# Kernel tuning notes

Hardware: AMD Instinct MI355X
Metric: run time of the kernel (lower is better)

The kernel has to match this reference:

```python
import jax, jax.numpy as jnp
import numpy as np

B, S, H, NH = 2, 2048, 1024, 16
P = H // NH

def setup_inputs() -> dict:
    key = jax.random.key(0)
    k1, k2, k3, k4 = jax.random.split(key, 4)
    x = jax.random.normal(k1, (B, S, H), dtype=jnp.float32)
    mask = jax.random.randint(k2, (B, S), 0, 2).astype(jnp.int32)
    # weights: (num_heads, 3, hidden, partial) -- the leading singleton dim of the
    # torch parameter is pure broadcast, dropped here.
    W = jax.random.normal(k3, (NH, 3, H, P), dtype=jnp.float32) * (1.0 / np.sqrt(H))
    Wl = jax.random.normal(k4, (H, H), dtype=jnp.float32) * (1.0 / np.sqrt(H))
    bl = jnp.zeros((H,), dtype=jnp.float32)
    return {"x": x, "mask": mask, "W": W, "Wl": Wl, "bl": bl}

def reference(x, mask, W, Wl, bl):
    nh, _, h, p = W.shape
    scale = 1.0 / np.sqrt(p)
    # kvq[b, t, n, s, p]; t=0 keys, t=1 values, t=2 queries (unbind order in source)
    kvq = jnp.einsum('bsh,nthp->btnsp', x, W)
    keys, values, queries = kvq[:, 0], kvq[:, 1], kvq[:, 2]  # each [B, NH, S, P]
    # NOTE: source computes keys @ queries^T -> scores[b,n,i,j] = k_i . q_j
    scores = jnp.einsum('bnip,bnjp->bnij', keys, queries) * scale
    # mask==0 zeroes out the LAST axis (query positions), exactly as the fancy-index write
    scores = jnp.where(mask[:, None, None, :] == 0, jnp.float32(-1e12), scores)
    # softmax over dim=2 (key axis), as in the source (Softmax(dim=2))
    w = jax.nn.softmax(scores, axis=2)
    out = jnp.einsum('bnij,bnjp->bnip', w, values)  # [B, NH, S, P]
    b, _, s, _ = out.shape
    hidden = out.transpose(0, 2, 1, 3).reshape(b, s, nh * p)  # concat heads
    return hidden @ Wl.T + bl
```

## Files before the change

kernel.cpp:

```cpp
#include <hip/hip_runtime.h>

#define B_ 2
#define S_ 2048
#define H_ 1024
#define NH_ 16
#define P_ 64

using f32x4 = __attribute__((ext_vector_type(4))) float;
using i32x4 = __attribute__((ext_vector_type(4))) int;
using f16   = _Float16;
using f16x8 = __attribute__((ext_vector_type(8))) f16;
using f16x4 = __attribute__((ext_vector_type(4))) f16;

static __device__ __forceinline__ f16x8 ldh8(const f16* p) { return *(const f16x8*)p; }
static __device__ __forceinline__ f32x4 ld4f(const float* p) { return *(const f32x4*)p; }

static __device__ __forceinline__ f32x4 mm16(f16x8 a, f16x8 b, f32x4 c) {
  return __builtin_amdgcn_mfma_f32_16x16x32_f16(a, b, c, 0, 0, 0);
}

__global__ __launch_bounds__(256) void tw_kernel(
    const float* __restrict__ W, f16* __restrict__ WtH)
{
  __shared__ float T[64 * 65];
  const int tid = threadIdx.x;
  const int nt = blockIdx.x >> 4;
  const int h0 = (blockIdx.x & 15) * 64;
  const float* src = W + (size_t)nt * H_ * P_ + (size_t)h0 * P_;
  #pragma unroll
  for (int r = 0; r < 4; ++r) {
    int idx = tid + r * 256;
    int h = idx >> 4, p4 = (idx & 15) << 2;
    f32x4 v = ld4f(src + (size_t)h * P_ + p4);
    #pragma unroll
    for (int i = 0; i < 4; ++i) T[(p4 + i) * 65 + h] = v[i];
  }
  __syncthreads();
  f16* dh = WtH + (size_t)nt * P_ * H_;
  #pragma unroll
  for (int r = 0; r < 4; ++r) {
    int idx = tid + r * 256;
    int p = idx >> 4, h4 = (idx & 15) << 2;
    f16x4 hv;
    #pragma unroll
    for (int i = 0; i < 4; ++i) hv[i] = (f16)T[p * 65 + h4 + i];
    *(f16x4*)(dh + (size_t)p * H_ + h0 + h4) = hv;
  }
}

__global__ __launch_bounds__(256) void swl_kernel(
    const float* __restrict__ Wl, f16* __restrict__ WlH)
{
  int idx = blockIdx.x * 256 + threadIdx.x;
  f32x4 v = ((const f32x4*)Wl)[idx];
  f16x4 h;
  #pragma unroll
  for (int i = 0; i < 4; ++i) h[i] = (f16)v[i];
  ((f16x4*)WlH)[idx] = h;
}

__global__ __launch_bounds__(256) void qkv_kernel(
    const float* __restrict__ x, const f16* __restrict__ WtH,
    f16* __restrict__ Kh, f16* __restrict__ Qh, f16* __restrict__ VTh)
{
  __shared__ f16 xls[2][64 * 64];

  int blk = blockIdx.x;
  const int st = blk & 31; blk >>= 5;
  const int n = blk & 15;
  const int b = blk >> 4;
  const int s0 = st * 64;
  const int tid = threadIdx.x;
  const int w = tid >> 6, lane = tid & 63, q = lane >> 4, fr = lane & 15;
  const int bn = b * NH_ + n;

  const int srow = tid >> 2, scc = tid & 3;
  const float* xsrc = x + ((size_t)b * S_ + s0 + srow) * H_ + 16 * scc;
  const int c0 = ((2 * scc) ^ (srow & 7)) * 8;
  const int c1 = ((2 * scc + 1) ^ (srow & 7)) * 8;

  auto stage = [&](int k0, int bs) {
    f32x4 v0 = ld4f(xsrc + k0),     v1 = ld4f(xsrc + k0 + 4);
    f32x4 v2 = ld4f(xsrc + k0 + 8), v3 = ld4f(xsrc + k0 + 12);
    f16x8 a, b2;
    #pragma unroll
    for (int e = 0; e < 4; ++e) {
      a[e] = (f16)v0[e];  a[e + 4] = (f16)v1[e];
      b2[e] = (f16)v2[e]; b2[e + 4] = (f16)v3[e];
    }
    *(f16x8*)&xls[bs][srow * 64 + c0] = a;
    *(f16x8*)&xls[bs][srow * 64 + c1] = b2;
  };

  const f16* WtK = WtH + ((size_t)(n * 3 + 0) * P_ + 16 * w + fr) * H_ + 8 * q;
  const f16* WtV = WtH + ((size_t)(n * 3 + 1) * P_ + 16 * w + fr) * H_ + 8 * q;
  const f16* WtQ = WtH + ((size_t)(n * 3 + 2) * P_ + 16 * w + fr) * H_ + 8 * q;

  f32x4 accK[4] = {}, accQ[4] = {}, accV[4] = {};

  stage(0, 0);
  for (int step = 0; step < 16; ++step) {
    __syncthreads();
    if (step < 15) stage((step + 1) * 64, (step + 1) & 1);
    const int bs = step & 1;
    const int k0 = step * 64;

    f16x8 xf[4][2];
    #pragma unroll
    for (int ss = 0; ss < 4; ++ss) {
      int row = 16 * ss + fr;
      #pragma unroll
      for (int ks = 0; ks < 2; ++ks) {
        int ch = ((q + 4 * ks) ^ (row & 7)) * 8;
        xf[ss][ks] = *(const f16x8*)&xls[bs][row * 64 + ch];
      }
    }
    f16x8 wk0 = ldh8(WtK + k0), wk1 = ldh8(WtK + k0 + 32);
    f16x8 wq0 = ldh8(WtQ + k0), wq1 = ldh8(WtQ + k0 + 32);
    f16x8 wv0 = ldh8(WtV + k0), wv1 = ldh8(WtV + k0 + 32);
    #pragma unroll
    for (int ss = 0; ss < 4; ++ss) {
      accK[ss] = mm16(wk0, xf[ss][0], accK[ss]);
      accK[ss] = mm16(wk1, xf[ss][1], accK[ss]);
      accQ[ss] = mm16(wq0, xf[ss][0], accQ[ss]);
      accQ[ss] = mm16(wq1, xf[ss][1], accQ[ss]);
      accV[ss] = mm16(xf[ss][0], wv0, accV[ss]);
      accV[ss] = mm16(xf[ss][1], wv1, accV[ss]);
    }
  }

  #pragma unroll
  for (int ss = 0; ss < 4; ++ss) {
    f16x4 hK, hQ;
    #pragma unroll
    for (int c = 0; c < 4; ++c) {
      hK[c] = (f16)accK[ss][c];
      hQ[c] = (f16)(accQ[ss][c] * 0.125f);
    }
    size_t off = ((size_t)bn * S_ + (s0 + 16 * ss + fr)) * P_ + 16 * w + 4 * q;
    *(f16x4*)(Kh + off) = hK;
    *(f16x4*)(Qh + off) = hQ;
  }
  #pragma unroll
  for (int ss = 0; ss < 4; ++ss) {
    f16x4 hV;
    #pragma unroll
    for (int c = 0; c < 4; ++c) hV[c] = (f16)accV[ss][c];
    size_t off = ((size_t)bn * P_ + (16 * w + fr)) * S_ + s0 + 16 * ss + 4 * q;
    *(f16x4*)(VTh + off) = hV;
  }
}

__global__ __launch_bounds__(256) void stats_kernel(
    const f16* __restrict__ Kh, const f16* __restrict__ Qh,
    float* __restrict__ csuminv)
{
  __shared__ float zbuf[2 * 64];
  const int tid = threadIdx.x;
  const int bid = blockIdx.x;
  const int j0 = (bid & 31) * 64;
  const int bn = bid >> 5;
  const int w = tid >> 6, lane = tid & 63, q = lane >> 4, fr = lane & 15;
  const int jb = 32 * (w & 1), ih = w >> 1, ib0 = 32 * ih;

  f16x8 qf[2][2];
  #pragma unroll
  for (int jt = 0; jt < 2; ++jt)
    #pragma unroll
    for (int ks = 0; ks < 2; ++ks)
      qf[jt][ks] = ldh8(Qh + ((size_t)bn * S_ + (j0 + jb + 16 * jt + fr)) * P_ + 8 * q + 32 * ks);

  f32x4 z[2] = {};
  f16x8 kA[2][2], kB[2][2];

  auto loadK = [&](f16x8 (&kf)[2][2], int i0) {
    #pragma unroll
    for (int it = 0; it < 2; ++it)
      #pragma unroll
      for (int ks = 0; ks < 2; ++ks)
        kf[it][ks] = ldh8(Kh + ((size_t)bn * S_ + (i0 + ib0 + 16 * it + fr)) * P_ + 8 * q + 32 * ks);
  };
  auto step = [&](f16x8 (&kf)[2][2]) {
    f32x4 sc[2][2] = {};
    #pragma unroll
    for (int ks = 0; ks < 2; ++ks)
      #pragma unroll
      for (int jt = 0; jt < 2; ++jt)
        #pragma unroll
        for (int it = 0; it < 2; ++it)
          sc[jt][it] = mm16(qf[jt][ks], kf[it][ks], sc[jt][it]);
    #pragma unroll
    for (int jt = 0; jt < 2; ++jt)
      #pragma unroll
      for (int c = 0; c < 4; ++c)
        z[jt][c] += __expf(sc[jt][0][c]) + __expf(sc[jt][1][c]);
  };

  loadK(kA, 0);
  for (int i0 = 0; i0 < S_; i0 += 128) {
    loadK(kB, i0 + 64);
    step(kA);
    loadK(kA, (i0 + 128) & (S_ - 1));
    step(kB);
  }

  #pragma unroll
  for (int msk = 1; msk <= 8; msk <<= 1)
    #pragma unroll
    for (int jt = 0; jt < 2; ++jt)
      #pragma unroll
      for (int c = 0; c < 4; ++c)
        z[jt][c] += __shfl_xor(z[jt][c], msk, 64);

  if (fr == 0) {
    #pragma unroll
    for (int jt = 0; jt < 2; ++jt)
      *(f32x4*)&zbuf[ih * 64 + jb + 16 * jt + 4 * q] = z[jt];
  }
  __syncthreads();
  if (tid < 64)
    csuminv[(size_t)bn * S_ + j0 + tid] = 1.0f / (zbuf[tid] + zbuf[64 + tid]);
}

__global__ __launch_bounds__(256) void scale_kernel(
    f16* __restrict__ VT, const float* __restrict__ csuminv,
    const int* __restrict__ mask, float* __restrict__ Cbuf)
{
  const int bid = blockIdx.x;
  const int bn = bid >> 4;
  const int b = bn >> 4;
  const int p = (bid & 15) * 4 + (threadIdx.x >> 6);
  const int lane = threadIdx.x & 63;
  f16* row = VT + ((size_t)bn * P_ + p) * S_;
  const float* zr = csuminv + (size_t)bn * S_;
  const int* mr = mask + (size_t)b * S_;
  float acc = 0.0f;
  #pragma unroll
  for (int k = 0; k < 4; ++k) {
    int s = (lane + 64 * k) * 8;
    f16x8 v = *(const f16x8*)(row + s);
    f32x4 z0 = ld4f(zr + s), z1 = ld4f(zr + s + 4);
    i32x4 m0 = *(const i32x4*)(mr + s), m1 = *(const i32x4*)(mr + s + 4);
    f16x8 o;
    #pragma unroll
    for (int e = 0; e < 4; ++e) {
      float fv = (float)v[e];
      if (m0[e] != 0) o[e] = (f16)(fv * z0[e]);
      else { o[e] = (f16)0.0f; acc += fv; }
      float fv2 = (float)v[e + 4];
      if (m1[e] != 0) o[e + 4] = (f16)(fv2 * z1[e]);
      else { o[e + 4] = (f16)0.0f; acc += fv2; }
    }
    *(f16x8*)(row + s) = o;
  }
  #pragma unroll
  for (int msk = 1; msk <= 32; msk <<= 1) acc += __shfl_xor(acc, msk, 64);
  if (lane == 0) Cbuf[bn * P_ + p] = acc * (1.0f / S_);
}

__global__ __launch_bounds__(256) void av_kernel(
    const f16* __restrict__ Kh, const f16* __restrict__ Qh,
    const f16* __restrict__ VT, const float* __restrict__ Cbuf,
    f16* __restrict__ hidh)
{
  __shared__ f16  elds[4][64 * 40];
  __shared__ float accl[64 * 68];
  const int tid = threadIdx.x;
  const int bid = blockIdx.x;
  const int i0 = (bid & 31) * 64;
  const int bn = bid >> 5;
  const int b = bn >> 4, n = bn & 15;
  const int w = tid >> 6, lane = tid & 63, q = lane >> 4, fr = lane & 15;
  f16* ew = &elds[w][0];

  f16x8 kf[4][2];
  #pragma unroll
  for (int it = 0; it < 4; ++it)
    #pragma unroll
    for (int ks = 0; ks < 2; ++ks)
      kf[it][ks] = ldh8(Kh + ((size_t)bn * S_ + (i0 + 16 * it + fr)) * P_ + 8 * q + 32 * ks);

  f32x4 opv[4][4] = {};

  for (int T = 0; T < S_ / 128; ++T) {
    const int j0 = T * 128 + w * 32;

    f16x8 aq[2][2];
    #pragma unroll
    for (int jt = 0; jt < 2; ++jt)
      #pragma unroll
      for (int ks = 0; ks < 2; ++ks)
        aq[jt][ks] = ldh8(Qh + ((size_t)bn * S_ + (j0 + 16 * jt + fr)) * P_ + 8 * q + 32 * ks);
    f16x8 va[4];
    #pragma unroll
    for (int pt = 0; pt < 4; ++pt)
      va[pt] = ldh8(VT + ((size_t)bn * P_ + (16 * pt + fr)) * S_ + j0 + 8 * q);

    #pragma unroll
    for (int it = 0; it < 4; ++it) {
      f32x4 s0 = {}, s1 = {};
      s0 = mm16(aq[0][0], kf[it][0], s0);
      s0 = mm16(aq[0][1], kf[it][1], s0);
      s1 = mm16(aq[1][0], kf[it][0], s1);
      s1 = mm16(aq[1][1], kf[it][1], s1);
      f16x4 e0, e1;
      #pragma unroll
      for (int c = 0; c < 4; ++c) {
        e0[c] = (f16)__expf(s0[c]);
        e1[c] = (f16)__expf(s1[c]);
      }
      *(f16x4*)(ew + (16 * it + fr) * 40 + 4 * q)      = e0;
      *(f16x4*)(ew + (16 * it + fr) * 40 + 16 + 4 * q) = e1;
    }

    #pragma unroll
    for (int it = 0; it < 4; ++it) {
      f16x8 ef = *(const f16x8*)(ew + (16 * it + fr) * 40 + 8 * q);
      #pragma unroll
      for (int pt = 0; pt < 4; ++pt)
        opv[pt][it] = mm16(va[pt], ef, opv[pt][it]);
    }
  }

  #pragma unroll
  for (int r = 0; r < 4; ++r) {
    __syncthreads();
    if (w == r) {
      #pragma unroll
      for (int it = 0; it < 4; ++it)
        #pragma unroll
        for (int pt = 0; pt < 4; ++pt) {
          float* a = &accl[(16 * it + fr) * 68 + 16 * pt + 4 * q];
          if (r == 0) *(f32x4*)a = opv[pt][it];
          else {
            f32x4 old = *(const f32x4*)a;
            #pragma unroll
            for (int c = 0; c < 4; ++c) old[c] += opv[pt][it][c];
            *(f32x4*)a = old;
          }
        }
    }
  }
  __syncthreads();

  const int ti = tid >> 2;
  const int tp = (tid & 3) << 4;
  const float* cb = Cbuf + bn * P_ + tp;
  f16* dst = hidh + ((size_t)b * S_ + (i0 + ti)) * H_ + n * P_ + tp;
  #pragma unroll
  for (int h = 0; h < 2; ++h) {
    f32x4 a0 = *(const f32x4*)&accl[ti * 68 + tp + 8 * h];
    f32x4 a1 = *(const f32x4*)&accl[ti * 68 + tp + 8 * h + 4];
    f32x4 c0 = ld4f(cb + 8 * h);
    f32x4 c1 = ld4f(cb + 8 * h + 4);
    f16x8 o;
    #pragma unroll
    for (int e = 0; e < 4; ++e) {
      o[e]     = (f16)(a0[e] + c0[e]);
      o[e + 4] = (f16)(a1[e] + c1[e]);
    }
    *(f16x8*)(dst + 8 * h) = o;
  }
}

__global__ __launch_bounds__(256) void final_kernel(
    const f16* __restrict__ hidh, const f16* __restrict__ WlH,
    const float* __restrict__ bl, float* __restrict__ out)
{
  __shared__ f16 hl[2][64 * 32];
  const int tid = threadIdx.x;
  const int ot = blockIdx.x & 15;
  const int rt = blockIdx.x >> 4;
  const int r0 = rt * 64, o0 = ot * 64;
  const int w = tid >> 6, lane = tid & 63, q = lane >> 4, fr = lane & 15;

  const int srow = tid >> 2, scc = tid & 3;
  const f16* hsrc = hidh + (size_t)(r0 + srow) * H_ + 8 * scc;
  const int saddr = srow * 32 + ((scc ^ (srow & 3)) * 8);

  auto stage = [&](int k0, int bufsel) {
    *(f16x8*)&hl[bufsel][saddr] = ldh8(hsrc + k0);
  };

  const f16* WlA = WlH + ((size_t)(o0 + 16 * w + fr)) * H_ + 8 * q;

  f32x4 acc[4] = {};

  stage(0, 0);
  for (int step = 0; step < 32; ++step) {
    __syncthreads();
    if (step < 31) stage((step + 1) * 32, (step + 1) & 1);
    const int bs = step & 1;
    const int k0 = step * 32;

    f16x8 bh[4];
    #pragma unroll
    for (int ss = 0; ss < 4; ++ss) {
      int addr = (16 * ss + fr) * 32 + ((q ^ (fr & 3)) * 8);
      bh[ss] = *(const f16x8*)&hl[bs][addr];
    }
    f16x8 ah = ldh8(WlA + k0);
    #pragma unroll
    for (int ss = 0; ss < 4; ++ss)
      acc[ss] = mm16(ah, bh[ss], acc[ss]);
  }

  const int o = o0 + 16 * w + 4 * q;
  f32x4 bv = ld4f(bl + o);
  #pragma unroll
  for (int ss = 0; ss < 4; ++ss) {
    f32x4 v;
    #pragma unroll
    for (int c = 0; c < 4; ++c) v[c] = acc[ss][c] + bv[c];
    *(f32x4*)(out + (size_t)(r0 + 16 * ss + fr) * H_ + o) = v;
  }
}

extern "C" void kernel_launch(void* const* d_in, const int* in_sizes, int n_in,
                              void* d_out, int out_size, void* d_ws, size_t ws_size,
                              hipStream_t stream) {
  const float* x    = (const float*)d_in[0];
  const int*   mask = (const int*)d_in[1];
  const float* W    = (const float*)d_in[2];
  const float* Wl   = (const float*)d_in[3];
  const float* bl   = (const float*)d_in[4];
  float* out = (float*)d_out;

  const size_t SZ  = (size_t)B_ * NH_ * S_ * P_;
  const size_t SZW = (size_t)NH_ * 3 * H_ * P_;
  const size_t SZL = (size_t)H_ * H_;
  const size_t SZC = (size_t)B_ * NH_ * S_;
  const size_t SZH = (size_t)B_ * S_ * H_;

  char* p = (char*)d_ws;
  f16*   Kh   = (f16*)p;  p += SZ * 2;
  f16*   Qh   = (f16*)p;  p += SZ * 2;
  f16*   VTh  = (f16*)p;  p += SZ * 2;
  f16*   WtH  = (f16*)p;  p += SZW * 2;
  f16*   WlH  = (f16*)p;  p += SZL * 2;
  f16*   hidh = (f16*)p;  p += SZH * 2;
  float* csuminv = (float*)p; p += SZC * 4;
  float* Cbuf    = (float*)p; p += (size_t)B_ * NH_ * P_ * 4;

  tw_kernel   <<<NH_ * 3 * (H_ / 64), 256, 0, stream>>>(W, WtH);
  swl_kernel  <<<(SZL / 4) / 256, 256, 0, stream>>>(Wl, WlH);
  qkv_kernel  <<<B_ * NH_ * (S_ / 64), 256, 0, stream>>>(x, WtH, Kh, Qh, VTh);
  stats_kernel<<<B_ * NH_ * (S_ / 64), 256, 0, stream>>>(Kh, Qh, csuminv);
  scale_kernel<<<B_ * NH_ * 16, 256, 0, stream>>>(VTh, csuminv, mask, Cbuf);
  av_kernel   <<<B_ * NH_ * (S_ / 64), 256, 0, stream>>>(
      Kh, Qh, VTh, Cbuf, hidh);
  final_kernel<<<(B_ * S_ / 64) * (H_ / 64), 256, 0, stream>>>(
      hidh, WlH, bl, out);
}
```

Measured before the change: 235.3 us.

## Use exp2 with prescaled queries, halve av tile rows, deepen final K-step

Folds log2(e) into the query scale so the softmax exponentials use exp2f instead of __expf in the stats and av kernels. The av kernel now handles 32 key rows per block instead of 64, doubling the grid for better occupancy at the cost of reloading Q and V tiles twice as often. The final GEMM stages 64-wide K chunks with an 8-way XOR swizzle, halving the loop trips and barriers while using more LDS per block.

New measurement: 288.5 us. 22.6% more time.

```diff
diff --git a/kernel.cpp b/kernel.cpp
--- a/kernel.cpp
+++ b/kernel.cpp
@@ -11,6 +11,8 @@
 using f16   = _Float16;
 using f16x8 = __attribute__((ext_vector_type(8))) f16;
 using f16x4 = __attribute__((ext_vector_type(4))) f16;
+
+#define QSCALE 0.18033688f
 
 static __device__ __forceinline__ f16x8 ldh8(const f16* p) { return *(const f16x8*)p; }
 static __device__ __forceinline__ f32x4 ld4f(const float* p) { return *(const f32x4*)p; }
@@ -135,7 +137,7 @@
     #pragma unroll
     for (int c = 0; c < 4; ++c) {
       hK[c] = (f16)accK[ss][c];
-      hQ[c] = (f16)(accQ[ss][c] * 0.125f);
+      hQ[c] = (f16)(accQ[ss][c] * QSCALE);
     }
     size_t off = ((size_t)bn * S_ + (s0 + 16 * ss + fr)) * P_ + 16 * w + 4 * q;
     *(f16x4*)(Kh + off) = hK;
@@ -193,7 +195,7 @@
     for (int jt = 0; jt < 2; ++jt)
       #pragma unroll
       for (int c = 0; c < 4; ++c)
-        z[jt][c] += __expf(sc[jt][0][c]) + __expf(sc[jt][1][c]);
+        z[jt][c] += exp2f(sc[jt][0][c]) + exp2f(sc[jt][1][c]);
   };
 
   loadK(kA, 0);
@@ -263,24 +265,24 @@
     const f16* __restrict__ VT, const float* __restrict__ Cbuf,
     f16* __restrict__ hidh)
 {
-  __shared__ f16  elds[4][64 * 40];
-  __shared__ float accl[64 * 68];
+  __shared__ f16  elds[4][32 * 40];
+  __shared__ float accl[32 * 68];
   const int tid = threadIdx.x;
   const int bid = blockIdx.x;
-  const int i0 = (bid & 31) * 64;
-  const int bn = bid >> 5;
+  const int i0 = (bid & 63) * 32;
+  const int bn = bid >> 6;
   const int b = bn >> 4, n = bn & 15;
   const int w = tid >> 6, lane = tid & 63, q = lane >> 4, fr = lane & 15;
   f16* ew = &elds[w][0];
 
-  f16x8 kf[4][2];
-  #pragma unroll
-  for (int it = 0; it < 4; ++it)
+  f16x8 kf[2][2];
+  #pragma unroll
+  for (int it = 0; it < 2; ++it)
     #pragma unroll
     for (int ks = 0; ks < 2; ++ks)
       kf[it][ks] = ldh8(Kh + ((size_t)bn * S_ + (i0 + 16 * it + fr)) * P_ + 8 * q + 32 * ks);
 
-  f32x4 opv[4][4] = {};
+  f32x4 opv[4][2] = {};
 
   for (int T = 0; T < S_ / 128; ++T) {
     const int j0 = T * 128 + w * 32;
@@ -297,7 +299,7 @@
       va[pt] = ldh8(VT + ((size_t)bn * P_ + (16 * pt + fr)) * S_ + j0 + 8 * q);
 
     #pragma unroll
-    for (int it = 0; it < 4; ++it) {
+    for (int it = 0; it < 2; ++it) {
       f32x4 s0 = {}, s1 = {};
       s0 = mm16(aq[0][0], kf[it][0], s0);
       s0 = mm16(aq[0][1], kf[it][1], s0);
@@ -306,15 +308,15 @@
       f16x4 e0, e1;
       #pragma unroll
       for (int c = 0; c < 4; ++c) {
-        e0[c] = (f16)__expf(s0[c]);
-        e1[c] = (f16)__expf(s1[c]);
+        e0[c] = (f16)exp2f(s0[c]);
+        e1[c] = (f16)exp2f(s1[c]);
       }
       *(f16x4*)(ew + (16 * it + fr) * 40 + 4 * q)      = e0;
       *(f16x4*)(ew + (16 * it + fr) * 40 + 16 + 4 * q) = e1;
     }
 
     #pragma unroll
-    for (int it = 0; it < 4; ++it) {
+    for (int it = 0; it < 2; ++it) {
       f16x8 ef = *(const f16x8*)(ew + (16 * it + fr) * 40 + 8 * q);
       #pragma unroll
       for (int pt = 0; pt < 4; ++pt)
@@ -327,7 +329,7 @@
     __syncthreads();
     if (w == r) {
       #pragma unroll
-      for (int it = 0; it < 4; ++it)
+      for (int it = 0; it < 2; ++it)
         #pragma unroll
         for (int pt = 0; pt < 4; ++pt) {
           float* a = &accl[(16 * it + fr) * 68 + 16 * pt + 4 * q];
@@ -343,31 +345,26 @@
   }
   __syncthreads();
 
-  const int ti = tid >> 2;
-  const int tp = (tid & 3) << 4;
-  const float* cb = Cbuf + bn * P_ + tp;
-  f16* dst = hidh + ((size_t)b * S_ + (i0 + ti)) * H_ + n * P_ + tp;
-  #pragma unroll
-  for (int h = 0; h < 2; ++h) {
-    f32x4 a0 = *(const f32x4*)&accl[ti * 68 + tp + 8 * h];
-    f32x4 a1 = *(const f32x4*)&accl[ti * 68 + tp + 8 * h + 4];
-    f32x4 c0 = ld4f(cb + 8 * h);
-    f32x4 c1 = ld4f(cb + 8 * h + 4);
-    f16x8 o;
-    #pragma unroll
-    for (int e = 0; e < 4; ++e) {
-      o[e]     = (f16)(a0[e] + c0[e]);
-      o[e + 4] = (f16)(a1[e] + c1[e]);
-    }
-    *(f16x8*)(dst + 8 * h) = o;
-  }
+  const int ti = tid >> 3;
+  const int tp = (tid & 7) << 3;
+  f32x4 a0 = *(const f32x4*)&accl[ti * 68 + tp];
+  f32x4 a1 = *(const f32x4*)&accl[ti * 68 + tp + 4];
+  f32x4 c0 = ld4f(Cbuf + bn * P_ + tp);
+  f32x4 c1 = ld4f(Cbuf + bn * P_ + tp + 4);
+  f16x8 o;
+  #pragma unroll
+  for (int e = 0; e < 4; ++e) {
+    o[e]     = (f16)(a0[e] + c0[e]);
+    o[e + 4] = (f16)(a1[e] + c1[e]);
+  }
+  *(f16x8*)(hidh + ((size_t)b * S_ + (i0 + ti)) * H_ + n * P_ + tp) = o;
 }
 
 __global__ __launch_bounds__(256) void final_kernel(
     const f16* __restrict__ hidh, const f16* __restrict__ WlH,
     const float* __restrict__ bl, float* __restrict__ out)
 {
-  __shared__ f16 hl[2][64 * 32];
+  __shared__ f16 hl[2][64 * 64];
   const int tid = threadIdx.x;
   const int ot = blockIdx.x & 15;
   const int rt = blockIdx.x >> 4;
@@ -375,11 +372,15 @@
   const int w = tid >> 6, lane = tid & 63, q = lane >> 4, fr = lane & 15;
 
   const int srow = tid >> 2, scc = tid & 3;
-  const f16* hsrc = hidh + (size_t)(r0 + srow) * H_ + 8 * scc;
-  const int saddr = srow * 32 + ((scc ^ (srow & 3)) * 8);
-
-  auto stage = [&](int k0, int bufsel) {
-    *(f16x8*)&hl[bufsel][saddr] = ldh8(hsrc + k0);
+  const f16* hsrc = hidh + (size_t)(r0 + srow) * H_ + 16 * scc;
+  const int c0 = ((2 * scc) ^ (srow & 7)) * 8;
+  const int c1 = ((2 * scc + 1) ^ (srow & 7)) * 8;
+
+  auto stage = [&](int k0, int bs) {
+    f16x8 a = ldh8(hsrc + k0);
+    f16x8 b2 = ldh8(hsrc + k0 + 8);
+    *(f16x8*)&hl[bs][srow * 64 + c0] = a;
+    *(f16x8*)&hl[bs][srow * 64 + c1] = b2;
   };
 
   const f16* WlA = WlH + ((size_t)(o0 + 16 * w + fr)) * H_ + 8 * q;
@@ -387,22 +388,29 @@
   f32x4 acc[4] = {};
 
   stage(0, 0);
-  for (int step = 0; step < 32; ++step) {
+  for (int step = 0; step < 16; ++step) {
     __syncthreads();
-    if (step < 31) stage((step + 1) * 32, (step + 1) & 1);
+    if (step < 15) stage((step + 1) * 64, (step + 1) & 1);
     const int bs = step & 1;
-    const int k0 = step * 32;
-
-    f16x8 bh[4];
+    const int k0 = step * 64;
+
+    f16x8 bh[4][2];
     #pragma unroll
     for (int ss = 0; ss < 4; ++ss) {
-      int addr = (16 * ss + fr) * 32 + ((q ^ (fr & 3)) * 8);
-      bh[ss] = *(const f16x8*)&hl[bs][addr];
-    }
-    f16x8 ah = ldh8(WlA + k0);
-    #pragma unroll
-    for (int ss = 0; ss < 4; ++ss)
-      acc[ss] = mm16(ah, bh[ss], acc[ss]);
+      int row = 16 * ss + fr;
+      #pragma unroll
+      for (int ks = 0; ks < 2; ++ks) {
+        int ch = ((q + 4 * ks) ^ (row & 7)) * 8;
+        bh[ss][ks] = *(const f16x8*)&hl[bs][row * 64 + ch];
+      }
+    }
+    f16x8 ah0 = ldh8(WlA + k0);
+    f16x8 ah1 = ldh8(WlA + k0 + 32);
+    #pragma unroll
+    for (int ss = 0; ss < 4; ++ss) {
+      acc[ss] = mm16(ah0, bh[ss][0], acc[ss]);
+      acc[ss] = mm16(ah1, bh[ss][1], acc[ss]);
+    }
   }
 
   const int o = o0 + 16 * w + 4 * q;
@@ -447,7 +455,7 @@
   qkv_kernel  <<<B_ * NH_ * (S_ / 64), 256, 0, stream>>>(x, WtH, Kh, Qh, VTh);
   stats_kernel<<<B_ * NH_ * (S_ / 64), 256, 0, stream>>>(Kh, Qh, csuminv);
   scale_kernel<<<B_ * NH_ * 16, 256, 0, stream>>>(VTh, csuminv, mask, Cbuf);
-  av_kernel   <<<B_ * NH_ * (S_ / 64), 256, 0, stream>>>(
+  av_kernel   <<<B_ * NH_ * (S_ / 32), 256, 0, stream>>>(
       Kh, Qh, VTh, Cbuf, hidh);
   final_kernel<<<(B_ * S_ / 64) * (H_ / 64), 256, 0, stream>>>(
       hidh, WlH, bl, out);
```
